# Optimization experiments

Measured on AMD Instinct MI355X. Metric: run time of the kernel, lower is better.

The kernel has to match this reference:

```python
import jax, jax.numpy as jnp
import numpy as np

B, T, D, H = 2, 2048, 512, 8
HD = D // H  # head_dim = 64


def setup_inputs() -> dict:
    key = jax.random.key(0)
    k1, k2, k3, k4 = jax.random.split(key, 4)
    scale = 1.0 / np.sqrt(D)
    x = jax.random.normal(k1, (B, T, D), dtype=jnp.float32)
    periods = jax.random.randint(k2, (B, H), 0, 64, dtype=jnp.int32)
    w_qkv = jax.random.normal(k3, (3 * D, D), dtype=jnp.float32) * scale
    b_qkv = jnp.zeros((3 * D,), dtype=jnp.float32)
    w_out = jax.random.normal(k4, (D, D), dtype=jnp.float32) * scale
    b_out = jnp.zeros((D,), dtype=jnp.float32)
    return {"x": x, "periods": periods, "w_qkv": w_qkv, "b_qkv": b_qkv,
            "w_out": w_out, "b_out": b_out}


def reference(x, periods, w_qkv, b_qkv, w_out, b_out):
    # qkv projection: (B,T,3D) -> (3,B,H,T,HD)
    qkv = x @ w_qkv.T + b_qkv
    qkv = qkv.reshape(B, T, 3, H, HD).transpose(2, 0, 3, 1, 4)
    q, k, v = qkv[0], qkv[1], qkv[2]

    # periodic-causal mask: valid iff j <= i and (i-j) % p == 0, p = max(period,1)
    i_idx = jnp.arange(T, dtype=jnp.int32)[:, None]   # (T,1)
    j_idx = jnp.arange(T, dtype=jnp.int32)[None, :]   # (1,T)
    diff = i_idx - j_idx                              # (T,T)
    p = jnp.maximum(periods, 1)[:, :, None, None]     # (B,H,1,1)
    valid = (diff >= 0) & ((diff % p) == 0)           # (B,H,T,T)

    scores = jnp.einsum('bhqd,bhkd->bhqk', q, k) / np.sqrt(HD)
    scores = jnp.where(valid, scores, jnp.finfo(scores.dtype).min)
    attn = jax.nn.softmax(scores, axis=-1)

    out = jnp.einsum('bhqk,bhkd->bhqd', attn, v)
    out = out.transpose(0, 2, 1, 3).reshape(B, T, D)
    return out @ w_out.T + b_out
```

## Files before the change

### kernel.cpp

```cpp
#include <hip/hip_runtime.h>
#include <math.h>

#define B_  2
#define T_  2048
#define D_  512
#define H_  8
#define HD_ 64
#define QKVS (3*D_)

typedef __bf16 bf16x8 __attribute__((ext_vector_type(8)));
typedef float  f32x4  __attribute__((ext_vector_type(4)));

__device__ inline unsigned short f2bf(float f) {
  unsigned int u = __float_as_uint(f);
  return (unsigned short)((u + 0x7FFFu + ((u >> 16) & 1u)) >> 16);
}
__device__ inline unsigned int pack2bf(float lo, float hi) {
  return (unsigned int)f2bf(lo) | ((unsigned int)f2bf(hi) << 16);
}

__global__ void cast_all(const float* __restrict__ x,
                         const float* __restrict__ wq,
                         const float* __restrict__ wo,
                         unsigned short* __restrict__ xb,
                         unsigned short* __restrict__ wqb,
                         unsigned short* __restrict__ wob) {
  const int n_x  = (B_ * T_ * D_) / 4;
  const int n_wq = (QKVS * D_) / 4;
  const int n_wo = (D_ * D_) / 4;
  int i = blockIdx.x * blockDim.x + threadIdx.x;
  const float* src; unsigned short* dst; int off;
  if (i < n_x)                    { src = x;  dst = xb;  off = i; }
  else if (i < n_x + n_wq)        { src = wq; dst = wqb; off = i - n_x; }
  else if (i < n_x + n_wq + n_wo) { src = wo; dst = wob; off = i - n_x - n_wq; }
  else return;
  float4 v = ((const float4*)src)[off];
  ushort4 o;
  o.x = f2bf(v.x); o.y = f2bf(v.y); o.z = f2bf(v.z); o.w = f2bf(v.w);
  ((ushort4*)dst)[off] = o;
}

template<int BF16OUT>
__global__ __launch_bounds__(256, 3)
void gemm_nt_bk128(const unsigned short* __restrict__ A,
                   const unsigned short* __restrict__ Bw,
                   const float* __restrict__ bias, void* __restrict__ Cv,
                   int M, int N, int K) {
  __shared__ short Asd[4][128 * 32];
  __shared__ short Bsd[4][64 * 32];

  const int tid = threadIdx.x;
  const int w   = tid >> 6;
  const int l   = tid & 63;
  const int wr  = w >> 1;
  const int wc  = w & 1;
  const int q   = l >> 4;
  const int ml  = l & 15;
  const int arow = l >> 2;
  const int kch  = (l & 3) * 8;

  const int rowbase = blockIdx.y * 128;
  const int colbase = blockIdx.x * 64;

  f32x4 acc[4][2] = {};

  for (int k0 = 0; k0 < K; k0 += 128) {
    __syncthreads();
    #pragma unroll
    for (int pnl = 0; pnl < 4; ++pnl) {
      const int kp = k0 + pnl * 32;
      #pragma unroll
      for (int s = 0; s < 2; ++s) {
        const unsigned short* g =
            A + (size_t)(rowbase + s * 64 + w * 16 + arow) * K + kp + kch;
        __builtin_amdgcn_global_load_lds(
            (const __attribute__((address_space(1))) void*)g,
            (__attribute__((address_space(3))) void*)
                &Asd[pnl][s * 2048 + w * 512], 16, 0, 0);
      }
      const unsigned short* g =
          Bw + (size_t)(colbase + w * 16 + arow) * K + kp + kch;
      __builtin_amdgcn_global_load_lds(
          (const __attribute__((address_space(1))) void*)g,
          (__attribute__((address_space(3))) void*)&Bsd[pnl][w * 512],
          16, 0, 0);
    }
    __syncthreads();

    #pragma unroll
    for (int pnl = 0; pnl < 4; ++pnl) {
      bf16x8 af[4], bfr[2];
      #pragma unroll
      for (int mi = 0; mi < 4; ++mi)
        af[mi] = *(const bf16x8*)&Asd[pnl][(wr * 64 + mi * 16 + ml) * 32 + q * 8];
      #pragma unroll
      for (int ni = 0; ni < 2; ++ni)
        bfr[ni] = *(const bf16x8*)&Bsd[pnl][(wc * 32 + ni * 16 + ml) * 32 + q * 8];
      #pragma unroll
      for (int mi = 0; mi < 4; ++mi)
        #pragma unroll
        for (int ni = 0; ni < 2; ++ni)
          acc[mi][ni] = __builtin_amdgcn_mfma_f32_16x16x32_bf16(
              af[mi], bfr[ni], acc[mi][ni], 0, 0, 0);
    }
  }

  #pragma unroll
  for (int mi = 0; mi < 4; ++mi) {
    #pragma unroll
    for (int ni = 0; ni < 2; ++ni) {
      const int col = colbase + wc * 32 + ni * 16 + ml;
      const float bv = bias[col];
      #pragma unroll
      for (int r = 0; r < 4; ++r) {
        const int row = rowbase + wr * 64 + mi * 16 + q * 4 + r;
        const float val = acc[mi][ni][r] + bv;
        if (BF16OUT)
          ((unsigned short*)Cv)[(size_t)row * N + col] = f2bf(val);
        else
          ((float*)Cv)[(size_t)row * N + col] = val;
      }
    }
  }
}

__global__ __launch_bounds__(512)
void attn_flash4(const unsigned short* __restrict__ qkv,
                 const int* __restrict__ periods,
                 unsigned short* __restrict__ ao) {
  const int bh = blockIdx.x, slot = 62 - blockIdx.y;
  int p = periods[bh]; if (p < 1) p = 1;
  const int g  = slot / p;
  const int r  = slot - g * p;
  const int L  = (T_ - 1 - r) / p + 1;
  const int q0 = g << 6;
  if (q0 >= L) return;
  const int b = bh >> 3, h = bh & 7;
  const int Lrem = L - q0;
  const int Nkb  = min(L, q0 + 64);

  const int tid  = threadIdx.x;
  const int w    = tid >> 6;
  const int wq   = w & 3;
  const int half = tid >> 8;
  const int tl   = tid & 255;
  const int lane = tid & 63;
  const int Q = lane >> 4, c = lane & 15;

  __shared__ __align__(16) unsigned short Qs[64 * 72];
  __shared__ __align__(16) unsigned short Ks[2][64 * 72];
  __shared__ __align__(16) unsigned short Vt[2][64 * 72];

  const size_t rowb = (size_t)b * T_ * QKVS + (size_t)h * HD_;

  {
    const int u = tid >> 3, ch4 = (tid & 7) * 8;
    const int t = q0 + min(u, Lrem - 1);
    const unsigned short* gq = qkv + rowb + (size_t)(r + t * p) * QKVS + ch4;
    *(int4*)&Qs[u * 72 + ch4] = *(const int4*)gq;
  }
  __syncthreads();
  bf16x8 qf[2];
  qf[0] = *(const bf16x8*)&Qs[(wq * 16 + c) * 72 + Q * 8];
  qf[1] = *(const bf16x8*)&Qs[(wq * 16 + c) * 72 + Q * 8 + 32];

  const int qb      = wq * 16;
  const int nqw     = min(16, Lrem - qb);
  const int qglob   = q0 + qb + c;
  const int mylastk = q0 + qb + 15;

  float m_run = -3.0e38f, l_run = 0.f;
  f32x4 o[4] = {};
  const size_t kb = rowb + D_;
  const size_t vb = rowb + 2 * D_;

  const int krow = tl >> 2, koff = (tl & 3) * 16;
  const int vkey = tl & 63, vd0 = ((tl >> 6) & 3) * 8;

  const int R     = (Nkb + 63) >> 6;
  const int RA    = (R + 1) >> 1;
  const int myR   = half ? (R - RA) : RA;
  const int kbase = half ? (RA << 6) : 0;

  int4 kp0, kp1, vp0, vp1;
  if (myR > 0) {
    const int tk = min(kbase + krow, Nkb - 1);
    const int tv = min(kbase + vkey, Nkb - 1);
    const unsigned short* gk = qkv + kb + (size_t)(r + tk * p) * QKVS + koff;
    const unsigned short* gv = qkv + vb + (size_t)(r + tv * p) * QKVS;
    kp0 = ((const int4*)gk)[0];
    kp1 = ((const int4*)gk)[1];
    vp0 = *(const int4*)(gv + vd0);
    vp1 = *(const int4*)(gv + vd0 + 32);
  }

  for (int rr = 0; rr < RA; ++rr) {
    const int k0 = kbase + (rr << 6);
    __syncthreads();
    if (rr < myR) {
      *(int4*)&Ks[half][krow * 72 + koff + 0] = kp0;
      *(int4*)&Ks[half][krow * 72 + koff + 8] = kp1;
      unsigned short vh0[8], vh1[8];
      *(int4*)vh0 = vp0;
      *(int4*)vh1 = vp1;
      #pragma unroll
      for (int j = 0; j < 8; ++j) {
        Vt[half][(vd0 + j) * 72 + vkey]      = vh0[j];
        Vt[half][(vd0 + 32 + j) * 72 + vkey] = vh1[j];
      }
    }
    __syncthreads();

    if (rr + 1 < myR) {
      const int tk = min(k0 + 64 + krow, Nkb - 1);
      const int tv = min(k0 + 64 + vkey, Nkb - 1);
      const unsigned short* gk = qkv + kb + (size_t)(r + tk * p) * QKVS + koff;
      const unsigned short* gv = qkv + vb + (size_t)(r + tv * p) * QKVS;
      kp0 = ((const int4*)gk)[0];
      kp1 = ((const int4*)gk)[1];
      vp0 = *(const int4*)(gv + vd0);
      vp1 = *(const int4*)(gv + vd0 + 32);
    }

    if (rr < myR && nqw > 0 && k0 <= mylastk) {
      float pvv[16];
      float tmax = -3.0e38f;
      #pragma unroll
      for (int mt = 0; mt < 4; ++mt) {
        if (k0 + mt * 16 <= mylastk) {
          bf16x8 a0 = *(const bf16x8*)&Ks[half][(mt * 16 + c) * 72 + Q * 8];
          bf16x8 a1 = *(const bf16x8*)&Ks[half][(mt * 16 + c) * 72 + Q * 8 + 32];
          f32x4 s = {};
          s = __builtin_amdgcn_mfma_f32_16x16x32_bf16(a0, qf[0], s, 0, 0, 0);
          s = __builtin_amdgcn_mfma_f32_16x16x32_bf16(a1, qf[1], s, 0, 0, 0);
          #pragma unroll
          for (int rg = 0; rg < 4; ++rg) {
            const int kk = k0 + mt * 16 + Q * 4 + rg;
            float v = s[rg] * 0.125f;
            v = (kk <= qglob) ? v : -3.0e38f;
            pvv[mt * 4 + rg] = v;
            tmax = fmaxf(tmax, v);
          }
        } else {
          #pragma unroll
          for (int rg = 0; rg < 4; ++rg) pvv[mt * 4 + rg] = -3.0e38f;
        }
      }

      tmax = fmaxf(tmax, __shfl_xor(tmax, 16));
      tmax = fmaxf(tmax, __shfl_xor(tmax, 32));
      const float m_new = fmaxf(m_run, tmax);
      const float alpha = __expf(m_run - m_new);
      float tsum = 0.f;
      #pragma unroll
      for (int i = 0; i < 16; ++i) {
        pvv[i] = __expf(pvv[i] - m_new);
        tsum += pvv[i];
      }
      tsum += __shfl_xor(tsum, 16);
      tsum += __shfl_xor(tsum, 32);
      l_run = l_run * alpha + tsum;
      m_run = m_new;

      bf16x8 pb[2];
      const int sq2 = (Q & 1) << 1;
      #pragma unroll
      for (int kc = 0; kc < 2; ++kc) {
        unsigned int pk0[2], pk1[2];
        pk0[0] = pack2bf(pvv[kc * 8 + 0], pvv[kc * 8 + 1]);
        pk0[1] = pack2bf(pvv[kc * 8 + 2], pvv[kc * 8 + 3]);
        pk1[0] = pack2bf(pvv[kc * 8 + 4], pvv[kc * 8 + 5]);
        pk1[1] = pack2bf(pvv[kc * 8 + 6], pvv[kc * 8 + 7]);
        int dw[4];
        #pragma unroll
        for (int d = 0; d < 4; ++d) {
          const int src = ((sq2 + (d >> 1)) << 4) + c;
          const int v0 = __shfl((int)pk0[d & 1], src);
          const int v1 = __shfl((int)pk1[d & 1], src);
          dw[d] = (Q >= 2) ? v1 : v0;
        }
        int4 bi = make_int4(dw[0], dw[1], dw[2], dw[3]);
        pb[kc] = *(bf16x8*)&bi;
      }

      #pragma unroll
      for (int ch = 0; ch < 4; ++ch)
        #pragma unroll
        for (int t2 = 0; t2 < 4; ++t2) o[ch][t2] *= alpha;
      #pragma unroll
      for (int kc = 0; kc < 2; ++kc) {
        if (k0 + kc * 32 <= mylastk) {
          #pragma unroll
          for (int ch = 0; ch < 4; ++ch) {
            bf16x8 af =
                *(const bf16x8*)&Vt[half][(ch * 16 + c) * 72 + kc * 32 + Q * 8];
            o[ch] = __builtin_amdgcn_mfma_f32_16x16x32_bf16(af, pb[kc], o[ch],
                                                            0, 0, 0);
          }
        }
      }
    }
  }

  __syncthreads();
  float* obuf = (float*)&Ks[0][0];
  float* mlb  = (float*)&Vt[0][0];
  if (half && nqw > 0) {
    float* ob = &obuf[(wq * 64 + lane) * 17];
    #pragma unroll
    for (int ch = 0; ch < 4; ++ch)
      #pragma unroll
      for (int t2 = 0; t2 < 4; ++t2) ob[ch * 4 + t2] = o[ch][t2];
    if (Q == 0) { mlb[wq * 32 + c] = m_run; mlb[wq * 32 + 16 + c] = l_run; }
  }
  __syncthreads();

  if (!half && nqw > 0 && c < nqw) {
    const float mB = mlb[wq * 32 + c];
    const float lB = mlb[wq * 32 + 16 + c];
    const float M  = fmaxf(m_run, mB);
    const float wA = __expf(m_run - M);
    const float wB = __expf(mB - M);
    const float invl = 1.f / (wA * l_run + wB * lB);
    const float* ob = &obuf[(wq * 64 + lane) * 17];
    const int tok = r + (q0 + qb + c) * p;
    unsigned int* dst =
        (unsigned int*)(ao + (size_t)(b * T_ + tok) * D_ + h * HD_);
    #pragma unroll
    for (int ch = 0; ch < 4; ++ch)
      #pragma unroll
      for (int rp = 0; rp < 2; ++rp) {
        const int dhalf = ch * 16 + Q * 4 + rp * 2;
        const float v0 =
            (wA * o[ch][rp * 2]     + wB * ob[ch * 4 + rp * 2])     * invl;
        const float v1 =
            (wA * o[ch][rp * 2 + 1] + wB * ob[ch * 4 + rp * 2 + 1]) * invl;
        dst[dhalf >> 1] = pack2bf(v0, v1);
      }
  }
}

extern "C" void kernel_launch(void* const* d_in, const int* in_sizes, int n_in,
                              void* d_out, int out_size, void* d_ws, size_t ws_size,
                              hipStream_t stream) {
  const float* x      = (const float*)d_in[0];
  const int*   period = (const int*)  d_in[1];
  const float* w_qkv  = (const float*)d_in[2];
  const float* b_qkv  = (const float*)d_in[3];
  const float* w_out  = (const float*)d_in[4];
  const float* b_out  = (const float*)d_in[5];
  float* out = (float*)d_out;

  const int M = B_ * T_;

  char* ws = (char*)d_ws;
  unsigned short* xb   = (unsigned short*)(ws);
  unsigned short* wqb  = (unsigned short*)(ws + (size_t)M * D_ * 2);
  unsigned short* wob  = (unsigned short*)(ws + (size_t)M * D_ * 2
                                              + (size_t)QKVS * D_ * 2);
  unsigned short* qkvb = (unsigned short*)(ws + (size_t)M * D_ * 2
                                              + (size_t)QKVS * D_ * 2
                                              + (size_t)D_ * D_ * 2);
  unsigned short* aob  = xb;

  {
    const int n4 = (M * D_ + QKVS * D_ + D_ * D_) / 4;
    cast_all<<<dim3((n4 + 255) / 256), dim3(256), 0, stream>>>(
        x, w_qkv, w_out, xb, wqb, wob);
  }

  gemm_nt_bk128<1><<<dim3(QKVS / 64, M / 128), dim3(256), 0, stream>>>(
      xb, wqb, b_qkv, qkvb, M, QKVS, D_);

  attn_flash4<<<dim3(16, 63), dim3(512), 0, stream>>>(qkvb, period, aob);

  gemm_nt_bk128<0><<<dim3(D_ / 64, M / 128), dim3(256), 0, stream>>>(
      aob, wob, b_out, out, M, D_, D_);
}
```

Baseline: 107.1 us.

## Fuse fp32-to-bf16 casts into GEMM loaders and drop separate cast kernel

Removes the standalone cast kernel that converted x, w_qkv and w_out to bf16. The GEMMs now stage fp32 tiles into LDS and convert to bf16 while building MFMA fragments. It also adds a block-index swizzle for L2 locality. This saves one launch and a full read/write pass over the inputs, at the cost of twice the global and LDS traffic per tile, more LDS per block, and conversion ALU inside the GEMM inner loop.

```diff
diff --git a/kernel.cpp b/kernel.cpp
--- a/kernel.cpp
+++ b/kernel.cpp
@@ -19,35 +19,23 @@
   return (unsigned int)f2bf(lo) | ((unsigned int)f2bf(hi) << 16);
 }
 
-__global__ void cast_all(const float* __restrict__ x,
-                         const float* __restrict__ wq,
-                         const float* __restrict__ wo,
-                         unsigned short* __restrict__ xb,
-                         unsigned short* __restrict__ wqb,
-                         unsigned short* __restrict__ wob) {
-  const int n_x  = (B_ * T_ * D_) / 4;
-  const int n_wq = (QKVS * D_) / 4;
-  const int n_wo = (D_ * D_) / 4;
-  int i = blockIdx.x * blockDim.x + threadIdx.x;
-  const float* src; unsigned short* dst; int off;
-  if (i < n_x)                    { src = x;  dst = xb;  off = i; }
-  else if (i < n_x + n_wq)        { src = wq; dst = wqb; off = i - n_x; }
-  else if (i < n_x + n_wq + n_wo) { src = wo; dst = wob; off = i - n_x - n_wq; }
-  else return;
-  float4 v = ((const float4*)src)[off];
-  ushort4 o;
-  o.x = f2bf(v.x); o.y = f2bf(v.y); o.z = f2bf(v.z); o.w = f2bf(v.w);
-  ((ushort4*)dst)[off] = o;
-}
-
-template<int BF16OUT>
+__device__ inline bf16x8 cvt8(const float* __restrict__ s) {
+  float4 a = *(const float4*)s;
+  float4 b = *(const float4*)(s + 4);
+  bf16x8 r;
+  r[0] = (__bf16)a.x; r[1] = (__bf16)a.y; r[2] = (__bf16)a.z; r[3] = (__bf16)a.w;
+  r[4] = (__bf16)b.x; r[5] = (__bf16)b.y; r[6] = (__bf16)b.z; r[7] = (__bf16)b.w;
+  return r;
+}
+
 __global__ __launch_bounds__(256, 3)
-void gemm_nt_bk128(const unsigned short* __restrict__ A,
-                   const unsigned short* __restrict__ Bw,
-                   const float* __restrict__ bias, void* __restrict__ Cv,
-                   int M, int N, int K) {
-  __shared__ short Asd[4][128 * 32];
-  __shared__ short Bsd[4][64 * 32];
+void gemm_qkv_f32(const float* __restrict__ A,
+                  const float* __restrict__ Bw,
+                  const float* __restrict__ bias,
+                  unsigned short* __restrict__ C,
+                  int M, int N, int K) {
+  __shared__ __align__(16) float Asf[2][128 * 32];
+  __shared__ __align__(16) float Bsf[2][64 * 32];
 
   const int tid = threadIdx.x;
   const int w   = tid >> 6;
@@ -56,46 +44,51 @@
   const int wc  = w & 1;
   const int q   = l >> 4;
   const int ml  = l & 15;
-  const int arow = l >> 2;
-  const int kch  = (l & 3) * 8;
-
-  const int rowbase = blockIdx.y * 128;
-  const int colbase = blockIdx.x * 64;
+  const int srow = tid >> 3;
+  const int scol = (tid & 7) * 4;
+
+  int flat = blockIdx.y * gridDim.x + blockIdx.x;
+  const int nb = gridDim.x * gridDim.y;
+  flat = (flat & 7) * (nb >> 3) + (flat >> 3);
+  const int bx = flat % gridDim.x, by = flat / gridDim.x;
+  const int rowbase = by * 128;
+  const int colbase = bx * 64;
 
   f32x4 acc[4][2] = {};
 
-  for (int k0 = 0; k0 < K; k0 += 128) {
-    __syncthreads();
-    #pragma unroll
-    for (int pnl = 0; pnl < 4; ++pnl) {
-      const int kp = k0 + pnl * 32;
-      #pragma unroll
-      for (int s = 0; s < 2; ++s) {
-        const unsigned short* g =
-            A + (size_t)(rowbase + s * 64 + w * 16 + arow) * K + kp + kch;
+  for (int k0 = 0; k0 < K; k0 += 64) {
+    __syncthreads();
+    #pragma unroll
+    for (int s = 0; s < 2; ++s) {
+      const int kp = k0 + s * 32;
+      #pragma unroll
+      for (int i = 0; i < 4; ++i) {
+        const float* g = A + (size_t)(rowbase + i * 32 + srow) * K + kp + scol;
         __builtin_amdgcn_global_load_lds(
             (const __attribute__((address_space(1))) void*)g,
             (__attribute__((address_space(3))) void*)
-                &Asd[pnl][s * 2048 + w * 512], 16, 0, 0);
-      }
-      const unsigned short* g =
-          Bw + (size_t)(colbase + w * 16 + arow) * K + kp + kch;
-      __builtin_amdgcn_global_load_lds(
-          (const __attribute__((address_space(1))) void*)g,
-          (__attribute__((address_space(3))) void*)&Bsd[pnl][w * 512],
-          16, 0, 0);
-    }
-    __syncthreads();
-
-    #pragma unroll
-    for (int pnl = 0; pnl < 4; ++pnl) {
+                ((char*)&Asf[s][0] + i * 4096 + w * 1024), 16, 0, 0);
+      }
+      #pragma unroll
+      for (int i = 0; i < 2; ++i) {
+        const float* g = Bw + (size_t)(colbase + i * 32 + srow) * K + kp + scol;
+        __builtin_amdgcn_global_load_lds(
+            (const __attribute__((address_space(1))) void*)g,
+            (__attribute__((address_space(3))) void*)
+                ((char*)&Bsf[s][0] + i * 4096 + w * 1024), 16, 0, 0);
+      }
+    }
+    __syncthreads();
+
+    #pragma unroll
+    for (int s = 0; s < 2; ++s) {
       bf16x8 af[4], bfr[2];
       #pragma unroll
       for (int mi = 0; mi < 4; ++mi)
-        af[mi] = *(const bf16x8*)&Asd[pnl][(wr * 64 + mi * 16 + ml) * 32 + q * 8];
+        af[mi] = cvt8(&Asf[s][(wr * 64 + mi * 16 + ml) * 32 + q * 8]);
       #pragma unroll
       for (int ni = 0; ni < 2; ++ni)
-        bfr[ni] = *(const bf16x8*)&Bsd[pnl][(wc * 32 + ni * 16 + ml) * 32 + q * 8];
+        bfr[ni] = cvt8(&Bsf[s][(wc * 32 + ni * 16 + ml) * 32 + q * 8]);
       #pragma unroll
       for (int mi = 0; mi < 4; ++mi)
         #pragma unroll
@@ -114,11 +107,93 @@
       #pragma unroll
       for (int r = 0; r < 4; ++r) {
         const int row = rowbase + wr * 64 + mi * 16 + q * 4 + r;
-        const float val = acc[mi][ni][r] + bv;
-        if (BF16OUT)
-          ((unsigned short*)Cv)[(size_t)row * N + col] = f2bf(val);
-        else
-          ((float*)Cv)[(size_t)row * N + col] = val;
+        C[(size_t)row * N + col] = f2bf(acc[mi][ni][r] + bv);
+      }
+    }
+  }
+}
+
+__global__ __launch_bounds__(256, 2)
+void gemm_out_mix(const unsigned short* __restrict__ A,
+                  const float* __restrict__ Bw,
+                  const float* __restrict__ bias,
+                  float* __restrict__ C,
+                  int M, int N, int K) {
+  __shared__ __align__(16) short Ash[4][128 * 32];
+  __shared__ __align__(16) float Bsf[4][64 * 32];
+
+  const int tid = threadIdx.x;
+  const int w   = tid >> 6;
+  const int l   = tid & 63;
+  const int wr  = w >> 1;
+  const int wc  = w & 1;
+  const int q   = l >> 4;
+  const int ml  = l & 15;
+  const int arow = tid >> 2, ach = (tid & 3) * 8;
+  const int srow = tid >> 3, scol = (tid & 7) * 4;
+
+  int flat = blockIdx.y * gridDim.x + blockIdx.x;
+  const int nb = gridDim.x * gridDim.y;
+  flat = (flat & 7) * (nb >> 3) + (flat >> 3);
+  const int bx = flat % gridDim.x, by = flat / gridDim.x;
+  const int rowbase = by * 128;
+  const int colbase = bx * 64;
+
+  f32x4 acc[4][2] = {};
+
+  for (int k0 = 0; k0 < K; k0 += 128) {
+    __syncthreads();
+    #pragma unroll
+    for (int s = 0; s < 4; ++s) {
+      const int kp = k0 + s * 32;
+      #pragma unroll
+      for (int i = 0; i < 2; ++i) {
+        const unsigned short* g =
+            A + (size_t)(rowbase + i * 64 + arow) * K + kp + ach;
+        __builtin_amdgcn_global_load_lds(
+            (const __attribute__((address_space(1))) void*)g,
+            (__attribute__((address_space(3))) void*)
+                ((char*)&Ash[s][0] + i * 4096 + w * 1024), 16, 0, 0);
+      }
+      #pragma unroll
+      for (int i = 0; i < 2; ++i) {
+        const float* g = Bw + (size_t)(colbase + i * 32 + srow) * K + kp + scol;
+        __builtin_amdgcn_global_load_lds(
+            (const __attribute__((address_space(1))) void*)g,
+            (__attribute__((address_space(3))) void*)
+                ((char*)&Bsf[s][0] + i * 4096 + w * 1024), 16, 0, 0);
+      }
+    }
+    __syncthreads();
+
+    #pragma unroll
+    for (int s = 0; s < 4; ++s) {
+      bf16x8 af[4], bfr[2];
+      #pragma unroll
+      for (int mi = 0; mi < 4; ++mi)
+        af[mi] = *(const bf16x8*)&Ash[s][(wr * 64 + mi * 16 + ml) * 32 + q * 8];
+      #pragma unroll
+      for (int ni = 0; ni < 2; ++ni)
+        bfr[ni] = cvt8(&Bsf[s][(wc * 32 + ni * 16 + ml) * 32 + q * 8]);
+      #pragma unroll
+      for (int mi = 0; mi < 4; ++mi)
+        #pragma unroll
+        for (int ni = 0; ni < 2; ++ni)
+          acc[mi][ni] = __builtin_amdgcn_mfma_f32_16x16x32_bf16(
+              af[mi], bfr[ni], acc[mi][ni], 0, 0, 0);
+    }
+  }
+
+  #pragma unroll
+  for (int mi = 0; mi < 4; ++mi) {
+    #pragma unroll
+    for (int ni = 0; ni < 2; ++ni) {
+      const int col = colbase + wc * 32 + ni * 16 + ml;
+      const float bv = bias[col];
+      #pragma unroll
+      for (int r = 0; r < 4; ++r) {
+        const int row = rowbase + wr * 64 + mi * 16 + q * 4 + r;
+        C[(size_t)row * N + col] = acc[mi][ni][r] + bv;
       }
     }
   }
@@ -354,26 +429,14 @@
   const int M = B_ * T_;
 
   char* ws = (char*)d_ws;
-  unsigned short* xb   = (unsigned short*)(ws);
-  unsigned short* wqb  = (unsigned short*)(ws + (size_t)M * D_ * 2);
-  unsigned short* wob  = (unsigned short*)(ws + (size_t)M * D_ * 2
-                                              + (size_t)QKVS * D_ * 2);
-  unsigned short* qkvb = (unsigned short*)(ws + (size_t)M * D_ * 2
-                                              + (size_t)QKVS * D_ * 2
-                                              + (size_t)D_ * D_ * 2);
-  unsigned short* aob  = xb;
-
-  {
-    const int n4 = (M * D_ + QKVS * D_ + D_ * D_) / 4;
-    cast_all<<<dim3((n4 + 255) / 256), dim3(256), 0, stream>>>(
-        x, w_qkv, w_out, xb, wqb, wob);
-  }
-
-  gemm_nt_bk128<1><<<dim3(QKVS / 64, M / 128), dim3(256), 0, stream>>>(
-      xb, wqb, b_qkv, qkvb, M, QKVS, D_);
+  unsigned short* qkvb = (unsigned short*)(ws);
+  unsigned short* aob  = (unsigned short*)(ws + (size_t)M * QKVS * 2);
+
+  gemm_qkv_f32<<<dim3(QKVS / 64, M / 128), dim3(256), 0, stream>>>(
+      x, w_qkv, b_qkv, qkvb, M, QKVS, D_);
 
   attn_flash4<<<dim3(16, 63), dim3(512), 0, stream>>>(qkvb, period, aob);
 
-  gemm_nt_bk128<0><<<dim3(D_ / 64, M / 128), dim3(256), 0, stream>>>(
-      aob, wob, b_out, out, M, D_, D_);
-}
+  gemm_out_mix<<<dim3(D_ / 64, M / 128), dim3(256), 0, stream>>>(
+      aob, w_out, b_out, out, M, D_, D_);
+}
```

Result: slower. 198.4 us (+85.2%).

## Fuse fp32-to-bf16 casts into GEMM tile loads and swizzle block order

Applied to the files above, without the earlier changes.

Removes the separate cast kernel. The GEMMs now read fp32 x and the weights directly and convert to bf16 while staging tiles into shared memory, which saves one launch and a round trip of bf16 copies through global memory. In exchange, the weights are re-read and re-converted as fp32 by every block, and those loads now go through registers instead of the direct global-to-LDS path. It also remaps block indices with a stride-8 swizzle to change the tile scheduling order, and moves the attention output to its own workspace buffer.

```diff
diff --git a/kernel.cpp b/kernel.cpp
--- a/kernel.cpp
+++ b/kernel.cpp
@@ -19,35 +19,21 @@
   return (unsigned int)f2bf(lo) | ((unsigned int)f2bf(hi) << 16);
 }
 
-__global__ void cast_all(const float* __restrict__ x,
-                         const float* __restrict__ wq,
-                         const float* __restrict__ wo,
-                         unsigned short* __restrict__ xb,
-                         unsigned short* __restrict__ wqb,
-                         unsigned short* __restrict__ wob) {
-  const int n_x  = (B_ * T_ * D_) / 4;
-  const int n_wq = (QKVS * D_) / 4;
-  const int n_wo = (D_ * D_) / 4;
-  int i = blockIdx.x * blockDim.x + threadIdx.x;
-  const float* src; unsigned short* dst; int off;
-  if (i < n_x)                    { src = x;  dst = xb;  off = i; }
-  else if (i < n_x + n_wq)        { src = wq; dst = wqb; off = i - n_x; }
-  else if (i < n_x + n_wq + n_wo) { src = wo; dst = wob; off = i - n_x - n_wq; }
-  else return;
-  float4 v = ((const float4*)src)[off];
-  ushort4 o;
-  o.x = f2bf(v.x); o.y = f2bf(v.y); o.z = f2bf(v.z); o.w = f2bf(v.w);
-  ((ushort4*)dst)[off] = o;
-}
-
-template<int BF16OUT>
+__device__ inline bf16x8 cvt8r(float4 a, float4 b) {
+  bf16x8 r;
+  r[0] = (__bf16)a.x; r[1] = (__bf16)a.y; r[2] = (__bf16)a.z; r[3] = (__bf16)a.w;
+  r[4] = (__bf16)b.x; r[5] = (__bf16)b.y; r[6] = (__bf16)b.z; r[7] = (__bf16)b.w;
+  return r;
+}
+
+template<int AF32, int BF16OUT>
 __global__ __launch_bounds__(256, 3)
-void gemm_nt_bk128(const unsigned short* __restrict__ A,
-                   const unsigned short* __restrict__ Bw,
+void gemm_nt_fused(const void* __restrict__ Av,
+                   const float* __restrict__ Bw,
                    const float* __restrict__ bias, void* __restrict__ Cv,
                    int M, int N, int K) {
-  __shared__ short Asd[4][128 * 32];
-  __shared__ short Bsd[4][64 * 32];
+  __shared__ __align__(16) short Asd[4][128 * 32];
+  __shared__ __align__(16) short Bsd[4][64 * 32];
 
   const int tid = threadIdx.x;
   const int w   = tid >> 6;
@@ -59,8 +45,18 @@
   const int arow = l >> 2;
   const int kch  = (l & 3) * 8;
 
-  const int rowbase = blockIdx.y * 128;
-  const int colbase = blockIdx.x * 64;
+  const int rs_row = tid >> 2;
+  const int rs_k   = (tid & 3) * 8;
+
+  int flat = blockIdx.y * gridDim.x + blockIdx.x;
+  const int nb = gridDim.x * gridDim.y;
+  flat = (flat & 7) * (nb >> 3) + (flat >> 3);
+  const int bx = flat % gridDim.x, by = flat / gridDim.x;
+  const int rowbase = by * 128;
+  const int colbase = bx * 64;
+
+  const float*          Af = (const float*)Av;
+  const unsigned short* Ab = (const unsigned short*)Av;
 
   f32x4 acc[4][2] = {};
 
@@ -69,21 +65,33 @@
     #pragma unroll
     for (int pnl = 0; pnl < 4; ++pnl) {
       const int kp = k0 + pnl * 32;
-      #pragma unroll
-      for (int s = 0; s < 2; ++s) {
-        const unsigned short* g =
-            A + (size_t)(rowbase + s * 64 + w * 16 + arow) * K + kp + kch;
-        __builtin_amdgcn_global_load_lds(
-            (const __attribute__((address_space(1))) void*)g,
-            (__attribute__((address_space(3))) void*)
-                &Asd[pnl][s * 2048 + w * 512], 16, 0, 0);
-      }
-      const unsigned short* g =
-          Bw + (size_t)(colbase + w * 16 + arow) * K + kp + kch;
-      __builtin_amdgcn_global_load_lds(
-          (const __attribute__((address_space(1))) void*)g,
-          (__attribute__((address_space(3))) void*)&Bsd[pnl][w * 512],
-          16, 0, 0);
+      if (AF32) {
+        #pragma unroll
+        for (int j = 0; j < 2; ++j) {
+          const int s   = j * 256 + tid;
+          const int row = s >> 2, ko = (s & 3) * 8;
+          const float* g = Af + (size_t)(rowbase + row) * K + kp + ko;
+          float4 v0 = ((const float4*)g)[0];
+          float4 v1 = ((const float4*)g)[1];
+          *(bf16x8*)&Asd[pnl][s * 8] = cvt8r(v0, v1);
+        }
+      } else {
+        #pragma unroll
+        for (int s = 0; s < 2; ++s) {
+          const unsigned short* g =
+              Ab + (size_t)(rowbase + s * 64 + w * 16 + arow) * K + kp + kch;
+          __builtin_amdgcn_global_load_lds(
+              (const __attribute__((address_space(1))) void*)g,
+              (__attribute__((address_space(3))) void*)
+                  &Asd[pnl][s * 2048 + w * 512], 16, 0, 0);
+        }
+      }
+      {
+        const float* g = Bw + (size_t)(colbase + rs_row) * K + kp + rs_k;
+        float4 v0 = ((const float4*)g)[0];
+        float4 v1 = ((const float4*)g)[1];
+        *(bf16x8*)&Bsd[pnl][tid * 8] = cvt8r(v0, v1);
+      }
     }
     __syncthreads();
 
@@ -354,26 +362,14 @@
   const int M = B_ * T_;
 
   char* ws = (char*)d_ws;
-  unsigned short* xb   = (unsigned short*)(ws);
-  unsigned short* wqb  = (unsigned short*)(ws + (size_t)M * D_ * 2);
-  unsigned short* wob  = (unsigned short*)(ws + (size_t)M * D_ * 2
-                                              + (size_t)QKVS * D_ * 2);
-  unsigned short* qkvb = (unsigned short*)(ws + (size_t)M * D_ * 2
-                                              + (size_t)QKVS * D_ * 2
-                                              + (size_t)D_ * D_ * 2);
-  unsigned short* aob  = xb;
-
-  {
-    const int n4 = (M * D_ + QKVS * D_ + D_ * D_) / 4;
-    cast_all<<<dim3((n4 + 255) / 256), dim3(256), 0, stream>>>(
-        x, w_qkv, w_out, xb, wqb, wob);
-  }
-
-  gemm_nt_bk128<1><<<dim3(QKVS / 64, M / 128), dim3(256), 0, stream>>>(
-      xb, wqb, b_qkv, qkvb, M, QKVS, D_);
+  unsigned short* qkvb = (unsigned short*)(ws);
+  unsigned short* aob  = (unsigned short*)(ws + (size_t)M * QKVS * 2);
+
+  gemm_nt_fused<1, 1><<<dim3(QKVS / 64, M / 128), dim3(256), 0, stream>>>(
+      x, w_qkv, b_qkv, qkvb, M, QKVS, D_);
 
   attn_flash4<<<dim3(16, 63), dim3(512), 0, stream>>>(qkvb, period, aob);
 
-  gemm_nt_bk128<0><<<dim3(D_ / 64, M / 128), dim3(256), 0, stream>>>(
-      aob, wob, b_out, out, M, D_, D_);
-}
+  gemm_nt_fused<0, 0><<<dim3(D_ / 64, M / 128), dim3(256), 0, stream>>>(
+      aob, w_out, b_out, out, M, D_, D_);
+}
```

New measurement: 109.1 us. Within noise of the previous version (+1.8%).
